# Kernel optimization log

Measured on AMD Instinct MI355X. Metric: run time of the kernel, lower is better.

The kernel has to match this reference:

```python
import jax, jax.numpy as jnp
import numpy as np

N = 100000   # nodes
D = 16       # fixed neighbor-set size (regular graph)
H = 128      # h_feats
L = 2        # num_iterations (stacked SAGEConv layers)
C = 10       # num_outputs


def setup_inputs() -> dict:
    key = jax.random.key(0)
    ks = jax.random.split(key, 20)
    s = 1.0 / np.sqrt(H)
    u = lambda k, shp: jax.random.uniform(k, shp, jnp.float32, -s, s)
    inp = {
        "h": jax.random.normal(ks[0], (N, H), jnp.float32),
        "nbr": jax.random.randint(ks[1], (N, D), 0, N, jnp.int32),
        # per-layer SAGEConv(lstm) params, stacked over L
        "lstm_Wih": u(ks[2], (L, 4 * H, H)),
        "lstm_Whh": u(ks[3], (L, 4 * H, H)),
        "lstm_b":   u(ks[4], (L, 4 * H)),   # b_ih + b_hh folded together
        "Wself":    u(ks[5], (L, H, H)),
        "bself":    u(ks[6], (L, H)),
        "Wneigh":   u(ks[7], (L, H, H)),
        "bneigh":   u(ks[8], (L, H)),
        "cls_W":  u(ks[9], (5, H, H)),
        "cls_b":  u(ks[10], (5, H)),
        "cls_oW": u(ks[11], (C, H)),
        "cls_ob": u(ks[12], (C,)),
        # cnf head: same but final Linear H->1
        "cnf_W":  u(ks[13], (5, H, H)),
        "cnf_b":  u(ks[14], (5, H)),
        "cnf_oW": u(ks[15], (1, H)),
        "cnf_ob": u(ks[16], (1,)),
    }
    return inp


def _sage_lstm_layer(h, nbr, Wih, Whh, b, Ws, bs, Wn, bn):
    """DGL SAGEConv with 'lstm' aggregator over a fixed-degree neighbor list.
    LSTM (PyTorch gate order i,f,g,o) runs over the D neighbors of every node;
    the final hidden state is the neighborhood aggregate."""
    hs0 = jnp.zeros((h.shape[0], H), h.dtype)
    cs0 = jnp.zeros_like(hs0)

    def step(carry, idx_row):            # idx_row: [N] neighbor ids at step t
        hs, cs = carry
        x = h[idx_row]                   # gather neighbor features [N, H]
        gates = x @ Wih.T + hs @ Whh.T + b
        i, f, g, o = jnp.split(gates, 4, axis=-1)
        cs = jax.nn.sigmoid(f) * cs + jax.nn.sigmoid(i) * jnp.tanh(g)
        hs = jax.nn.sigmoid(o) * jnp.tanh(cs)
        return (hs, cs), None

    (h_neigh, _), _ = jax.lax.scan(step, (hs0, cs0), nbr.T)  # scan over D steps
    return jax.nn.relu(h @ Ws.T + bs + h_neigh @ Wn.T + bn)


def _mlp_head(x, W, bvec, oW, ob):
    for i in range(5):
        x = jax.nn.relu(x @ W[i].T + bvec[i])   # Dropout(0.2) is identity in eval
    return x @ oW.T + ob


def reference(h, nbr, lstm_Wih, lstm_Whh, lstm_b, Wself, bself, Wneigh, bneigh,
              cls_W, cls_b, cls_oW, cls_ob, cnf_W, cnf_b, cnf_oW, cnf_ob):
    for layer in range(L):
        h = _sage_lstm_layer(h, nbr, lstm_Wih[layer], lstm_Whh[layer], lstm_b[layer],
                             Wself[layer], bself[layer], Wneigh[layer], bneigh[layer])
    o = _mlp_head(h, cls_W, cls_b, cls_oW, cls_ob)   # [N, C]
    l = _mlp_head(h, cnf_W, cnf_b, cnf_oW, cnf_ob)   # [N, 1]
    return (o, h, l)
```

## Files before the change

kernel.cpp:

```cpp
#include <hip/hip_runtime.h>
#include <stdint.h>


typedef __attribute__((ext_vector_type(8))) short short8_t;
typedef __attribute__((ext_vector_type(4))) float float4_t;
typedef __attribute__((ext_vector_type(4))) unsigned uint4_t;
typedef _Float16 half8_t __attribute__((ext_vector_type(8)));
typedef _Float16 half4_t __attribute__((ext_vector_type(4)));

#define NNODES 100000
#define DNB 16
#define LOSCALE 32768.0f
#define LOINV   3.0517578125e-5f

__device__ __forceinline__ float fsigf(float x) {
    return __builtin_amdgcn_rcpf(1.f + __expf(-x));
}
__device__ __forceinline__ float ftanhf(float x) {
    return 1.f - 2.f * __builtin_amdgcn_rcpf(1.f + __expf(2.f * x));
}
__device__ __forceinline__ unsigned f2b(float f) {
    unsigned u = __float_as_uint(f);
    return (u + 0x7FFFu + ((u >> 16) & 1u)) >> 16;
}
__device__ __forceinline__ float blo(unsigned u) { return __uint_as_float(u << 16); }
__device__ __forceinline__ float bhi(unsigned u) { return __uint_as_float(u & 0xFFFF0000u); }
__device__ __forceinline__ void splitf8(const float* __restrict__ p, short8_t& hi, short8_t& lo) {
    float4_t a = *(const float4_t*)p;
    float4_t b = *(const float4_t*)(p + 4);
#pragma unroll
    for (int j = 0; j < 8; ++j) {
        float x = j < 4 ? a[j] : b[j - 4];
        unsigned hb = f2b(x);
        float hf = __uint_as_float(hb << 16);
        unsigned lb = f2b(x - hf);
        hi[j] = (short)hb;
        lo[j] = (short)lb;
    }
}
__device__ __forceinline__ short8_t cvtb8(const float* __restrict__ p) {
    float4_t a = *(const float4_t*)p;
    float4_t b = *(const float4_t*)(p + 4);
    short8_t r;
    r[0] = (short)f2b(a[0]); r[1] = (short)f2b(a[1]);
    r[2] = (short)f2b(a[2]); r[3] = (short)f2b(a[3]);
    r[4] = (short)f2b(b[0]); r[5] = (short)f2b(b[1]);
    r[6] = (short)f2b(b[2]); r[7] = (short)f2b(b[3]);
    return r;
}

__global__ __launch_bounds__(256) void xgemm_split(
    const float* __restrict__ A, const float* __restrict__ B,
    const float* __restrict__ bias, _Float16* __restrict__ Chi,
    char* __restrict__ Clo)
{
    const int tid  = threadIdx.x;
    const int wave = tid >> 6, lane = tid & 63;
    const int l15  = lane & 15, quad = lane >> 4;
    const int r0   = blockIdx.y * 64 + wave * 16;
    const int c0   = blockIdx.x * 64;

    int arow = r0 + l15;
    if (arow >= NNODES) arow = NNODES - 1;

    float4_t acc[4];
#pragma unroll
    for (int ct = 0; ct < 4; ++ct) acc[ct] = (float4_t){0.f, 0.f, 0.f, 0.f};

#pragma unroll
    for (int kc = 0; kc < 4; ++kc) {
        const int kk = kc * 32 + quad * 8;
        short8_t ah, al;
        splitf8(A + (size_t)arow * 128 + kk, ah, al);
#pragma unroll
        for (int ct = 0; ct < 4; ++ct) {
            short8_t bh, bl;
            splitf8(B + (size_t)(c0 + ct * 16 + l15) * 128 + kk, bh, bl);
            acc[ct] = __builtin_amdgcn_mfma_f32_16x16x32_bf16(ah, bh, acc[ct], 0, 0, 0);
            acc[ct] = __builtin_amdgcn_mfma_f32_16x16x32_bf16(ah, bl, acc[ct], 0, 0, 0);
            acc[ct] = __builtin_amdgcn_mfma_f32_16x16x32_bf16(al, bh, acc[ct], 0, 0, 0);
        }
    }

#pragma unroll
    for (int ct = 0; ct < 4; ++ct) {
        int c = c0 + ct * 16 + l15;
        float bb = bias[c];
        const int jj = c & 127, gg = c >> 7;
#pragma unroll
        for (int r = 0; r < 4; ++r) {
            int rowo = r0 + quad * 4 + r;
            if (rowo < NNODES) {
                float v = acc[ct][r] + bb;
                _Float16 hi = (_Float16)v;
                float res = v - (float)hi;
                int q = (int)rintf(res * LOSCALE);
                q = q > 127 ? 127 : (q < -127 ? -127 : q);
                Chi[(size_t)rowo * 512 + jj * 4 + gg] = hi;
                Clo[(size_t)rowo * 512 + jj * 4 + gg] = (char)q;
            }
        }
    }
}

__global__ __launch_bounds__(512, 2) void lstm_comb(
    const _Float16* __restrict__ Xhi, const char* __restrict__ Xlo,
    const int* __restrict__ nbr, const float* __restrict__ Whh,
    const float* hin, const float* __restrict__ Ws,
    const float* __restrict__ Wn, const float* __restrict__ bs,
    const float* __restrict__ bn, float* hout)
{
    __shared__ short hsAhi[64 * 136], hsAlo[64 * 136];
    __shared__ short hsBhi[64 * 136], hsBlo[64 * 136];
    __shared__ int   nbrs[64 * 17];

    const int tid  = threadIdx.x;
    const int wave = tid >> 6, lane = tid & 63;
    const int l15  = lane & 15, quad = lane >> 4;
    const int n0   = blockIdx.x * 64;
    const int jb   = wave * 16;
    const int xoff = jb * 4 + quad * 16;

    for (int i = tid; i < 64 * 136 / 2; i += 512) {
        ((unsigned*)hsAhi)[i] = 0;
        ((unsigned*)hsAlo)[i] = 0;
    }
    for (int i = tid; i < 64 * DNB; i += 512) {
        int node = n0 + (i >> 4);
        if (node >= NNODES) node = NNODES - 1;
        nbrs[(i >> 4) * 17 + (i & 15)] = nbr[node * DNB + (i & 15)];
    }

    short8_t whi[4][4], wlo[4][4];
#pragma unroll
    for (int g = 0; g < 4; ++g)
#pragma unroll
        for (int kc = 0; kc < 4; ++kc)
            splitf8(Whh + (size_t)(g * 128 + jb + l15) * 128 + kc * 32 + quad * 8,
                    whi[g][kc], wlo[g][kc]);

    float cs[4][4], nh[4][4];
#pragma unroll
    for (int a = 0; a < 4; ++a)
#pragma unroll
        for (int b = 0; b < 4; ++b) { cs[a][b] = 0.f; nh[a][b] = 0.f; }

    __syncthreads();

#define XV(nt, r, g)                                                                \
    ((float)(((r) * 4 + (g)) < 8 ? xh0[nt][(r) * 4 + (g)] : xh1[nt][(r) * 4 + (g) - 8]) \
     + (float)((signed char)(xl4[nt][(r)] >> ((g) * 8))) * LOINV)

#define LSTM_STEP(rdHi, rdLo, wrHi, wrLo, T)                                        \
    {                                                                               \
        half8_t xh0[4], xh1[4]; uint4_t xl4[4];                                     \
        _Pragma("unroll")                                                           \
        for (int nt = 0; nt < 4; ++nt) {                                            \
            int gi = nbrs[(nt * 16 + l15) * 17 + (T)];                              \
            size_t xb = (size_t)gi * 512 + xoff;                                    \
            xh0[nt] = *(const half8_t*)(Xhi + xb);                                  \
            xh1[nt] = *(const half8_t*)(Xhi + xb + 8);                              \
            xl4[nt] = *(const uint4_t*)(Xlo + xb);                                  \
        }                                                                           \
        _Pragma("unroll")                                                           \
        for (int nt = 0; nt < 4; ++nt) {                                            \
            short8_t hfh[4], hfl[4];                                                \
            _Pragma("unroll")                                                       \
            for (int kc = 0; kc < 4; ++kc) {                                        \
                hfh[kc] = *(const short8_t*)&(rdHi)[(nt * 16 + l15) * 136 + kc * 32 + quad * 8]; \
                hfl[kc] = *(const short8_t*)&(rdLo)[(nt * 16 + l15) * 136 + kc * 32 + quad * 8]; \
            }                                                                       \
            float4_t ac[4];                                                         \
            _Pragma("unroll")                                                       \
            for (int g = 0; g < 4; ++g) {                                           \
                float4_t a = (float4_t){0.f, 0.f, 0.f, 0.f};                        \
                _Pragma("unroll")                                                   \
                for (int kc = 0; kc < 4; ++kc) {                                    \
                    a = __builtin_amdgcn_mfma_f32_16x16x32_bf16(whi[g][kc], hfh[kc], a, 0, 0, 0); \
                    a = __builtin_amdgcn_mfma_f32_16x16x32_bf16(whi[g][kc], hfl[kc], a, 0, 0, 0); \
                    a = __builtin_amdgcn_mfma_f32_16x16x32_bf16(wlo[g][kc], hfh[kc], a, 0, 0, 0); \
                }                                                                   \
                ac[g] = a;                                                          \
            }                                                                       \
            _Pragma("unroll")                                                       \
            for (int r = 0; r < 4; ++r) {                                           \
                float iv = ac[0][r] + XV(nt, r, 0);                                 \
                float fv = ac[1][r] + XV(nt, r, 1);                                 \
                float gv = ac[2][r] + XV(nt, r, 2);                                 \
                float ov = ac[3][r] + XV(nt, r, 3);                                 \
                float c = fsigf(fv) * cs[nt][r] + fsigf(iv) * ftanhf(gv);           \
                cs[nt][r] = c;                                                      \
                nh[nt][r] = fsigf(ov) * ftanhf(c);                                  \
            }                                                                       \
        }                                                                           \
        _Pragma("unroll")                                                           \
        for (int nt = 0; nt < 4; ++nt) {                                            \
            unsigned hb[4], lb[4];                                                  \
            _Pragma("unroll")                                                       \
            for (int r = 0; r < 4; ++r) {                                           \
                float v = nh[nt][r];                                                \
                hb[r] = f2b(v);                                                     \
                lb[r] = f2b(v - __uint_as_float(hb[r] << 16));                      \
            }                                                                       \
            uint2 ph, pl;                                                           \
            ph.x = hb[0] | (hb[1] << 16); ph.y = hb[2] | (hb[3] << 16);             \
            pl.x = lb[0] | (lb[1] << 16); pl.y = lb[2] | (lb[3] << 16);             \
            const int o = (nt * 16 + l15) * 136 + jb + quad * 4;                    \
            *(uint2*)&(wrHi)[o] = ph;                                               \
            *(uint2*)&(wrLo)[o] = pl;                                               \
        }                                                                           \
        __syncthreads();                                                            \
    }

    for (int tp = 0; tp < 8; ++tp) {
        LSTM_STEP(hsAhi, hsAlo, hsBhi, hsBlo, 2 * tp);
        LSTM_STEP(hsBhi, hsBlo, hsAhi, hsAlo, 2 * tp + 1);
    }
#undef LSTM_STEP
#undef XV

    const int ng = wave & 3, ch = wave >> 2;
    const int nodeA = n0 + ng * 16 + l15;
    const int nclA  = nodeA < NNODES ? nodeA : NNODES - 1;
    short8_t ahh[4], ahl[4], anh[4], anl[4];
#pragma unroll
    for (int kc = 0; kc < 4; ++kc) {
        splitf8(hin + (size_t)nclA * 128 + kc * 32 + quad * 8, ahh[kc], ahl[kc]);
        anh[kc] = *(const short8_t*)&hsAhi[(ng * 16 + l15) * 136 + kc * 32 + quad * 8];
        anl[kc] = *(const short8_t*)&hsAlo[(ng * 16 + l15) * 136 + kc * 32 + quad * 8];
    }
    __syncthreads();

#pragma unroll
    for (int ct = 0; ct < 4; ++ct) {
        const int ctg = ch * 4 + ct;
        float4_t acc = (float4_t){0.f, 0.f, 0.f, 0.f};
#pragma unroll
        for (int kc = 0; kc < 4; ++kc) {
            const int kk = kc * 32 + quad * 8;
            short8_t bh, bl;
            splitf8(Ws + (size_t)(ctg * 16 + l15) * 128 + kk, bh, bl);
            acc = __builtin_amdgcn_mfma_f32_16x16x32_bf16(ahh[kc], bh, acc, 0, 0, 0);
            acc = __builtin_amdgcn_mfma_f32_16x16x32_bf16(ahh[kc], bl, acc, 0, 0, 0);
            acc = __builtin_amdgcn_mfma_f32_16x16x32_bf16(ahl[kc], bh, acc, 0, 0, 0);
            splitf8(Wn + (size_t)(ctg * 16 + l15) * 128 + kk, bh, bl);
            acc = __builtin_amdgcn_mfma_f32_16x16x32_bf16(anh[kc], bh, acc, 0, 0, 0);
            acc = __builtin_amdgcn_mfma_f32_16x16x32_bf16(anh[kc], bl, acc, 0, 0, 0);
            acc = __builtin_amdgcn_mfma_f32_16x16x32_bf16(anl[kc], bh, acc, 0, 0, 0);
        }
        const int c = ctg * 16 + l15;
        const float bb = bs[c] + bn[c];
#pragma unroll
        for (int r = 0; r < 4; ++r) {
            int rowo = n0 + ng * 16 + quad * 4 + r;
            if (rowo < NNODES) {
                float v = acc[r] + bb;
                hout[(size_t)rowo * 128 + c] = v > 0.f ? v : 0.f;
            }
        }
    }
}

__global__ __launch_bounds__(256) void headgemm_b(
    const float* __restrict__ A32, const short* __restrict__ A16,
    const float* __restrict__ Bc, const float* __restrict__ Bn,
    const float* __restrict__ bc, const float* __restrict__ bn,
    short* __restrict__ C, int afmt)
{
    const int tid  = threadIdx.x;
    const int wave = tid >> 6, lane = tid & 63;
    const int l15  = lane & 15, quad = lane >> 4;
    const int r0   = blockIdx.x * 64 + wave * 16;
    const int c0   = blockIdx.y * 64;

    const float* Bw = (r0 < NNODES) ? Bc : Bn;
    const float* bw = (r0 < NNODES) ? bc : bn;
    int arow = r0 + l15;
    if (afmt && arow >= NNODES) arow -= NNODES;

    float4_t acc[4];
#pragma unroll
    for (int ct = 0; ct < 4; ++ct) acc[ct] = (float4_t){0.f, 0.f, 0.f, 0.f};

#pragma unroll
    for (int kc = 0; kc < 4; ++kc) {
        const int kk = kc * 32 + quad * 8;
        short8_t af = afmt ? cvtb8(A32 + (size_t)arow * 128 + kk)
                           : *(const short8_t*)(A16 + (size_t)arow * 128 + kk);
#pragma unroll
        for (int ct = 0; ct < 4; ++ct) {
            short8_t bf = cvtb8(Bw + (size_t)(c0 + ct * 16 + l15) * 128 + kk);
            acc[ct] = __builtin_amdgcn_mfma_f32_16x16x32_bf16(af, bf, acc[ct], 0, 0, 0);
        }
    }

#pragma unroll
    for (int ct = 0; ct < 4; ++ct) {
        int c = c0 + ct * 16 + l15;
        float bb = bw[c];
#pragma unroll
        for (int r = 0; r < 4; ++r) {
            int rowo = r0 + quad * 4 + r;
            float v = acc[ct][r] + bb;
            if (v < 0.f) v = 0.f;
            C[(size_t)rowo * 128 + c] = (short)f2b(v);
        }
    }
}

__global__ __launch_bounds__(256) void final_b(
    const short* __restrict__ xin, const float* __restrict__ W,
    const float* __restrict__ b, float* __restrict__ out, int C)
{
    int idx = blockIdx.x * blockDim.x + threadIdx.x;
    if (idx >= NNODES * C) return;
    int n = idx / C, c = idx - n * C;
    const short* xr = xin + (size_t)n * 128;
    const float* wr = W + (size_t)c * 128;
    float acc = b[c];
#pragma unroll
    for (int i = 0; i < 16; ++i) {
        uint4 xv = *(const uint4*)(xr + i * 8);
        const float* w = wr + i * 8;
        acc += blo(xv.x) * w[0] + bhi(xv.x) * w[1]
             + blo(xv.y) * w[2] + bhi(xv.y) * w[3]
             + blo(xv.z) * w[4] + bhi(xv.z) * w[5]
             + blo(xv.w) * w[6] + bhi(xv.w) * w[7];
    }
    out[idx] = acc;
}

extern "C" void kernel_launch(void* const* d_in, const int* in_sizes, int n_in,
                              void* d_out, int out_size, void* d_ws, size_t ws_size,
                              hipStream_t stream)
{
    const float* h0     = (const float*)d_in[0];
    const int*   nbr    = (const int*)d_in[1];
    const float* Wih    = (const float*)d_in[2];
    const float* Whh    = (const float*)d_in[3];
    const float* lb     = (const float*)d_in[4];
    const float* Wself  = (const float*)d_in[5];
    const float* bself  = (const float*)d_in[6];
    const float* Wneigh = (const float*)d_in[7];
    const float* bneigh = (const float*)d_in[8];
    const float* clsW   = (const float*)d_in[9];
    const float* clsb   = (const float*)d_in[10];
    const float* clsoW  = (const float*)d_in[11];
    const float* clsob  = (const float*)d_in[12];
    const float* cnfW   = (const float*)d_in[13];
    const float* cnfb   = (const float*)d_in[14];
    const float* cnfoW  = (const float*)d_in[15];
    const float* cnfob  = (const float*)d_in[16];

    char* ws = (char*)d_ws;
    _Float16* Xhi = (_Float16*)ws;
    char*     Xlo = ws + 102400000;
    short*    actA = (short*)ws;
    short*    actB = (short*)(ws + 51200000);

    float* out = (float*)d_out;
    float* oC  = out;
    float* hO  = out + 1000000;
    float* oL  = out + 13800000;

    dim3 gx(8, 1563);
    dim3 gl(1563);
    dim3 gh(3125, 2);

    xgemm_split<<<gx, dim3(256), 0, stream>>>(h0, Wih, lb, Xhi, Xlo);
    lstm_comb<<<gl, dim3(512), 0, stream>>>(Xhi, Xlo, nbr, Whh, h0,
                                            Wself, Wneigh, bself, bneigh, hO);
    xgemm_split<<<gx, dim3(256), 0, stream>>>(hO, Wih + 65536, lb + 512, Xhi, Xlo);
    lstm_comb<<<gl, dim3(512), 0, stream>>>(Xhi, Xlo, nbr, Whh + 65536, hO,
                                            Wself + 16384, Wneigh + 16384,
                                            bself + 128, bneigh + 128, hO);

    headgemm_b<<<gh, dim3(256), 0, stream>>>(hO, nullptr, clsW, cnfW, clsb, cnfb, actA, 1);
    short* cur = actA; short* nxt = actB;
    for (int i = 1; i < 5; ++i) {
        headgemm_b<<<gh, dim3(256), 0, stream>>>(nullptr, cur, clsW + i * 16384, cnfW + i * 16384,
                                                 clsb + i * 128, cnfb + i * 128, nxt, 0);
        short* tv = cur; cur = nxt; nxt = tv;
    }
    final_b<<<dim3((NNODES * 10 + 255) / 256), dim3(256), 0, stream>>>(cur, clsoW, clsob, oC, 10);
    final_b<<<dim3((NNODES + 255) / 256), dim3(256), 0, stream>>>(cur + (size_t)NNODES * 128,
                                                                  cnfoW, cnfob, oL, 1);
}
```

Baseline: 3.322 ms.

## Fuse both MLP heads into one LDS-resident kernel; use packed bf16 conversion

Replaces the chain of per-layer head GEMM launches and the two final projection kernels with a single kernel. Each block keeps a 64-row activation tile in LDS across all five layers of both heads and stages each layer's weights in LDS. This removes the global round-trips of the intermediate activations and several launches, at the cost of weight reconversion per block and extra barriers. Separately, scalar bf16 rounding is replaced by the packed v_cvt_pk_bf16_f32 instruction in the split conversion used by the input GEMM and in cvtb8.

New measurement: 2.920 ms. -12.1%, faster.

```diff
diff --git a/kernel.cpp b/kernel.cpp
--- a/kernel.cpp
+++ b/kernel.cpp
@@ -6,7 +6,6 @@
 typedef __attribute__((ext_vector_type(4))) float float4_t;
 typedef __attribute__((ext_vector_type(4))) unsigned uint4_t;
 typedef _Float16 half8_t __attribute__((ext_vector_type(8)));
-typedef _Float16 half4_t __attribute__((ext_vector_type(4)));
 
 #define NNODES 100000
 #define DNB 16
@@ -38,15 +37,33 @@
         lo[j] = (short)lb;
     }
 }
+__device__ __forceinline__ unsigned cvtpk(float lo, float hi) {
+    unsigned r;
+    asm("v_cvt_pk_bf16_f32 %0, %1, %2" : "=v"(r) : "v"(lo), "v"(hi));
+    return r;
+}
+__device__ __forceinline__ void splitf8_pk(const float* __restrict__ p, short8_t& hi, short8_t& lo) {
+    float4_t a = *(const float4_t*)p;
+    float4_t b = *(const float4_t*)(p + 4);
+    unsigned h0 = cvtpk(a[0], a[1]), h1 = cvtpk(a[2], a[3]);
+    unsigned h2 = cvtpk(b[0], b[1]), h3 = cvtpk(b[2], b[3]);
+    unsigned l0 = cvtpk(a[0] - blo(h0), a[1] - bhi(h0));
+    unsigned l1 = cvtpk(a[2] - blo(h1), a[3] - bhi(h1));
+    unsigned l2 = cvtpk(b[0] - blo(h2), b[1] - bhi(h2));
+    unsigned l3 = cvtpk(b[2] - blo(h3), b[3] - bhi(h3));
+    union { uint4_t u; short8_t s; } ch, cl;
+    ch.u = (uint4_t){h0, h1, h2, h3};
+    cl.u = (uint4_t){l0, l1, l2, l3};
+    hi = ch.s;
+    lo = cl.s;
+}
 __device__ __forceinline__ short8_t cvtb8(const float* __restrict__ p) {
     float4_t a = *(const float4_t*)p;
     float4_t b = *(const float4_t*)(p + 4);
-    short8_t r;
-    r[0] = (short)f2b(a[0]); r[1] = (short)f2b(a[1]);
-    r[2] = (short)f2b(a[2]); r[3] = (short)f2b(a[3]);
-    r[4] = (short)f2b(b[0]); r[5] = (short)f2b(b[1]);
-    r[6] = (short)f2b(b[2]); r[7] = (short)f2b(b[3]);
-    return r;
+    union { uint4_t u; short8_t s; } c;
+    c.u = (uint4_t){cvtpk(a[0], a[1]), cvtpk(a[2], a[3]),
+                    cvtpk(b[0], b[1]), cvtpk(b[2], b[3])};
+    return c.s;
 }
 
 __global__ __launch_bounds__(256) void xgemm_split(
@@ -71,11 +88,11 @@
     for (int kc = 0; kc < 4; ++kc) {
         const int kk = kc * 32 + quad * 8;
         short8_t ah, al;
-        splitf8(A + (size_t)arow * 128 + kk, ah, al);
+        splitf8_pk(A + (size_t)arow * 128 + kk, ah, al);
 #pragma unroll
         for (int ct = 0; ct < 4; ++ct) {
             short8_t bh, bl;
-            splitf8(B + (size_t)(c0 + ct * 16 + l15) * 128 + kk, bh, bl);
+            splitf8_pk(B + (size_t)(c0 + ct * 16 + l15) * 128 + kk, bh, bl);
             acc[ct] = __builtin_amdgcn_mfma_f32_16x16x32_bf16(ah, bh, acc[ct], 0, 0, 0);
             acc[ct] = __builtin_amdgcn_mfma_f32_16x16x32_bf16(ah, bl, acc[ct], 0, 0, 0);
             acc[ct] = __builtin_amdgcn_mfma_f32_16x16x32_bf16(al, bh, acc[ct], 0, 0, 0);
@@ -261,73 +278,120 @@
     }
 }
 
-__global__ __launch_bounds__(256) void headgemm_b(
-    const float* __restrict__ A32, const short* __restrict__ A16,
-    const float* __restrict__ Bc, const float* __restrict__ Bn,
-    const float* __restrict__ bc, const float* __restrict__ bn,
-    short* __restrict__ C, int afmt)
+__global__ __launch_bounds__(256) void heads_fused(
+    const float* __restrict__ hsrc,
+    const float* __restrict__ clsW, const float* __restrict__ clsb,
+    const float* __restrict__ clsoW, const float* __restrict__ clsob,
+    const float* __restrict__ cnfW, const float* __restrict__ cnfb,
+    const float* __restrict__ cnfoW, const float* __restrict__ cnfob,
+    float* __restrict__ oC, float* __restrict__ oL)
 {
+    __shared__ short xb[64 * 132];
+    __shared__ short wb[128 * 132];
+
     const int tid  = threadIdx.x;
     const int wave = tid >> 6, lane = tid & 63;
     const int l15  = lane & 15, quad = lane >> 4;
-    const int r0   = blockIdx.x * 64 + wave * 16;
-    const int c0   = blockIdx.y * 64;
-
-    const float* Bw = (r0 < NNODES) ? Bc : Bn;
-    const float* bw = (r0 < NNODES) ? bc : bn;
-    int arow = r0 + l15;
-    if (afmt && arow >= NNODES) arow -= NNODES;
-
-    float4_t acc[4];
-#pragma unroll
-    for (int ct = 0; ct < 4; ++ct) acc[ct] = (float4_t){0.f, 0.f, 0.f, 0.f};
-
-#pragma unroll
-    for (int kc = 0; kc < 4; ++kc) {
-        const int kk = kc * 32 + quad * 8;
-        short8_t af = afmt ? cvtb8(A32 + (size_t)arow * 128 + kk)
-                           : *(const short8_t*)(A16 + (size_t)arow * 128 + kk);
-#pragma unroll
-        for (int ct = 0; ct < 4; ++ct) {
-            short8_t bf = cvtb8(Bw + (size_t)(c0 + ct * 16 + l15) * 128 + kk);
-            acc[ct] = __builtin_amdgcn_mfma_f32_16x16x32_bf16(af, bf, acc[ct], 0, 0, 0);
-        }
-    }
-
-#pragma unroll
-    for (int ct = 0; ct < 4; ++ct) {
-        int c = c0 + ct * 16 + l15;
-        float bb = bw[c];
-#pragma unroll
-        for (int r = 0; r < 4; ++r) {
-            int rowo = r0 + quad * 4 + r;
-            float v = acc[ct][r] + bb;
-            if (v < 0.f) v = 0.f;
-            C[(size_t)rowo * 128 + c] = (short)f2b(v);
-        }
-    }
-}
-
-__global__ __launch_bounds__(256) void final_b(
-    const short* __restrict__ xin, const float* __restrict__ W,
-    const float* __restrict__ b, float* __restrict__ out, int C)
-{
-    int idx = blockIdx.x * blockDim.x + threadIdx.x;
-    if (idx >= NNODES * C) return;
-    int n = idx / C, c = idx - n * C;
-    const short* xr = xin + (size_t)n * 128;
-    const float* wr = W + (size_t)c * 128;
-    float acc = b[c];
-#pragma unroll
-    for (int i = 0; i < 16; ++i) {
-        uint4 xv = *(const uint4*)(xr + i * 8);
-        const float* w = wr + i * 8;
-        acc += blo(xv.x) * w[0] + bhi(xv.x) * w[1]
-             + blo(xv.y) * w[2] + bhi(xv.y) * w[3]
-             + blo(xv.z) * w[4] + bhi(xv.z) * w[5]
-             + blo(xv.w) * w[6] + bhi(xv.w) * w[7];
-    }
-    out[idx] = acc;
+    const int n0   = blockIdx.x * 64;
+
+    {
+        int row = tid >> 2, cb = (tid & 3) * 32;
+        int rsrc = n0 + row; if (rsrc >= NNODES) rsrc = NNODES - 1;
+        const float* src = hsrc + (size_t)rsrc * 128 + cb;
+#pragma unroll
+        for (int i = 0; i < 4; ++i)
+            *(short8_t*)&xb[row * 132 + cb + i * 8] = cvtb8(src + i * 8);
+    }
+
+    for (int head = 0; head < 2; ++head) {
+        const float* W  = head ? cnfW : clsW;
+        const float* bv = head ? cnfb : clsb;
+
+        if (head == 1) {
+            __syncthreads();
+            int row = tid >> 2, cb = (tid & 3) * 32;
+            int rsrc = n0 + row; if (rsrc >= NNODES) rsrc = NNODES - 1;
+            const float* src = hsrc + (size_t)rsrc * 128 + cb;
+#pragma unroll
+            for (int i = 0; i < 4; ++i)
+                *(short8_t*)&xb[row * 132 + cb + i * 8] = cvtb8(src + i * 8);
+        }
+
+        for (int l = 0; l < 5; ++l) {
+            __syncthreads();
+            short8_t af[4];
+#pragma unroll
+            for (int kc = 0; kc < 4; ++kc)
+                af[kc] = *(const short8_t*)&xb[(wave * 16 + l15) * 132 + kc * 32 + quad * 8];
+            const float* Wl = W + (size_t)l * 16384;
+#pragma unroll
+            for (int i = 0; i < 8; ++i) {
+                int e = i * 2048 + tid * 8;
+                int r = e >> 7, c = e & 127;
+                *(short8_t*)&wb[r * 132 + c] = cvtb8(Wl + e);
+            }
+            __syncthreads();
+#pragma unroll
+            for (int ct = 0; ct < 8; ++ct) {
+                float4_t acc = (float4_t){0.f, 0.f, 0.f, 0.f};
+#pragma unroll
+                for (int kc = 0; kc < 4; ++kc) {
+                    short8_t bf = *(const short8_t*)&wb[(ct * 16 + l15) * 132 + kc * 32 + quad * 8];
+                    acc = __builtin_amdgcn_mfma_f32_16x16x32_bf16(af[kc], bf, acc, 0, 0, 0);
+                }
+                int c = ct * 16 + l15;
+                float bb = bv[l * 128 + c];
+#pragma unroll
+                for (int r = 0; r < 4; ++r) {
+                    float v = acc[r] + bb;
+                    v = v > 0.f ? v : 0.f;
+                    xb[(wave * 16 + quad * 4 + r) * 132 + c] = (short)f2b(v);
+                }
+            }
+        }
+
+        __syncthreads();
+        short8_t af[4];
+#pragma unroll
+        for (int kc = 0; kc < 4; ++kc)
+            af[kc] = *(const short8_t*)&xb[(wave * 16 + l15) * 132 + kc * 32 + quad * 8];
+        if (head == 0) {
+            int wr = l15 < 10 ? l15 : 9;
+            float4_t acc = (float4_t){0.f, 0.f, 0.f, 0.f};
+#pragma unroll
+            for (int kc = 0; kc < 4; ++kc) {
+                short8_t bh, bl;
+                splitf8(clsoW + (size_t)wr * 128 + kc * 32 + quad * 8, bh, bl);
+                acc = __builtin_amdgcn_mfma_f32_16x16x32_bf16(af[kc], bh, acc, 0, 0, 0);
+                acc = __builtin_amdgcn_mfma_f32_16x16x32_bf16(af[kc], bl, acc, 0, 0, 0);
+            }
+            if (l15 < 10) {
+                float bb = clsob[l15];
+#pragma unroll
+                for (int r = 0; r < 4; ++r) {
+                    int row = n0 + wave * 16 + quad * 4 + r;
+                    if (row < NNODES) oC[(size_t)row * 10 + l15] = acc[r] + bb;
+                }
+            }
+        } else {
+            float4_t acc = (float4_t){0.f, 0.f, 0.f, 0.f};
+#pragma unroll
+            for (int kc = 0; kc < 4; ++kc) {
+                short8_t bh, bl;
+                splitf8(cnfoW + kc * 32 + quad * 8, bh, bl);
+                acc = __builtin_amdgcn_mfma_f32_16x16x32_bf16(af[kc], bh, acc, 0, 0, 0);
+                acc = __builtin_amdgcn_mfma_f32_16x16x32_bf16(af[kc], bl, acc, 0, 0, 0);
+            }
+            if (l15 == 0) {
+                float bb = cnfob[0];
+#pragma unroll
+                for (int r = 0; r < 4; ++r) {
+                    int row = n0 + wave * 16 + quad * 4 + r;
+                    if (row < NNODES) oL[row] = acc[r] + bb;
+                }
+            }
+        }
+    }
 }
 
 extern "C" void kernel_launch(void* const* d_in, const int* in_sizes, int n_in,
@@ -355,8 +419,6 @@
     char* ws = (char*)d_ws;
     _Float16* Xhi = (_Float16*)ws;
     char*     Xlo = ws + 102400000;
-    short*    actA = (short*)ws;
-    short*    actB = (short*)(ws + 51200000);
 
     float* out = (float*)d_out;
     float* oC  = out;
@@ -365,7 +427,7 @@
 
     dim3 gx(8, 1563);
     dim3 gl(1563);
-    dim3 gh(3125, 2);
+    dim3 gf(1563);
 
     xgemm_split<<<gx, dim3(256), 0, stream>>>(h0, Wih, lb, Xhi, Xlo);
     lstm_comb<<<gl, dim3(512), 0, stream>>>(Xhi, Xlo, nbr, Whh, h0,
@@ -375,14 +437,6 @@
                                             Wself + 16384, Wneigh + 16384,
                                             bself + 128, bneigh + 128, hO);
 
-    headgemm_b<<<gh, dim3(256), 0, stream>>>(hO, nullptr, clsW, cnfW, clsb, cnfb, actA, 1);
-    short* cur = actA; short* nxt = actB;
-    for (int i = 1; i < 5; ++i) {
-        headgemm_b<<<gh, dim3(256), 0, stream>>>(nullptr, cur, clsW + i * 16384, cnfW + i * 16384,
-                                                 clsb + i * 128, cnfb + i * 128, nxt, 0);
-        short* tv = cur; cur = nxt; nxt = tv;
-    }
-    final_b<<<dim3((NNODES * 10 + 255) / 256), dim3(256), 0, stream>>>(cur, clsoW, clsob, oC, 10);
-    final_b<<<dim3((NNODES + 255) / 256), dim3(256), 0, stream>>>(cur + (size_t)NNODES * 128,
-                                                                  cnfoW, cnfob, oL, 1);
-}
+    heads_fused<<<gf, dim3(256), 0, stream>>>(hO, clsW, clsb, clsoW, clsob,
+                                              cnfW, cnfb, cnfoW, cnfob, oC, oL);
+}
```
